# Performance work log

Measured on AMD Instinct MI355X. Metric: run time of the kernel, lower is better.

The kernel has to match this reference:

```python
import jax, jax.numpy as jnp
import numpy as np

B, SQ, SK = 8, 2048, 2048
QE = KE = VE = HID = 1024
NORM = HID ** 0.5


def setup_inputs() -> dict:
    key0 = jax.random.key(0)
    ks = jax.random.split(key0, 9)
    s = 1.0 / np.sqrt(HID)
    return {
        "key": jax.random.normal(ks[0], (B, SK, KE), dtype=jnp.float32),
        "query": jax.random.normal(ks[1], (B, SQ, QE), dtype=jnp.float32),
        "mask": jax.random.randint(ks[2], (B, SQ, SK), 0, 2, dtype=jnp.int32),
        # nn.Linear params: W has shape [out, in], y = x @ W.T + b
        "Wq": jax.random.uniform(ks[3], (HID, QE), jnp.float32, -s, s),
        "bq": jax.random.uniform(ks[4], (HID,), jnp.float32, -s, s),
        "Wk": jax.random.uniform(ks[5], (HID, KE), jnp.float32, -s, s),
        "bk": jax.random.uniform(ks[6], (HID,), jnp.float32, -s, s),
        "Wv": jax.random.uniform(ks[7], (HID, VE), jnp.float32, -s, s),
        "bv": jax.random.uniform(ks[8], (HID,), jnp.float32, -s, s),
    }


def reference(key, query, mask, Wq, bq, Wk, bk, Wv, bv):
    # QKV projections (note: value projection is applied to `key`, as in the original)
    q = jnp.einsum('bse,he->bsh', query, Wq) + bq   # [B,SQ,H]
    k = jnp.einsum('bse,he->bsh', key, Wk) + bk     # [B,SK,H]
    v = jnp.einsum('bse,he->bsh', key, Wv) + bv     # [B,SK,H]
    # scores + mask (0 -> -inf) in one fused pass
    score = jnp.einsum('bqh,bkh->bqk', q, k) / NORM  # [B,SQ,SK]
    score = jnp.where(mask == 0, -jnp.inf, score)
    score = jax.nn.softmax(score, axis=-1)
    # NaN cleanup for fully-masked rows (score.data[score != score] = 0)
    score = jnp.where(jnp.isnan(score), 0.0, score)
    output = jnp.einsum('bqk,bkh->bqh', score, v)    # [B,SQ,H]
    return (output, score)
```

## Files before the change

### kernel.cpp

```cpp
#include <hip/hip_runtime.h>
#include <hip/hip_bf16.h>

typedef __bf16 bf16;
typedef __bf16 bf16x8 __attribute__((ext_vector_type(8)));
typedef float  f32x4  __attribute__((ext_vector_type(4)));
typedef int    i32x4  __attribute__((ext_vector_type(4)));

#define TK 32
#define FB_TM 128
#define FB_TN 128
#define LDS_PAD 40

typedef __attribute__((address_space(3))) void       lds_t;
typedef __attribute__((address_space(1))) const void gbl_t;
__device__ __forceinline__ void async16(const void* g, void* l) {
    __builtin_amdgcn_global_load_lds((gbl_t*)g, (lds_t*)l, 16, 0, 0);
}

template<typename TC, int BIAS, int NTC>
__global__ __launch_bounds__(256, 2)
void gemm_bt(const bf16* __restrict__ A, const bf16* __restrict__ B,
             TC* __restrict__ C, const float* __restrict__ bias,
             int K, int lda, int ldb, int ldc,
             long sA, long sB, long sC)
{
    constexpr int BM  = 256, BN = 128;
    constexpr int ASZ = BM * TK;
    constexpr int BSZ = BN * TK;
    constexpr int BUFE = ASZ + BSZ;
    __shared__ bf16 lds[3 * BUFE];

    const int gx = gridDim.x, gy = gridDim.y;
    int lin = blockIdx.x + gx * (blockIdx.y + gy * blockIdx.z);
    const int cpx = (gx * gy * gridDim.z) >> 3;
    lin = (lin & 7) * cpx + (lin >> 3);
    const int bx  = lin % gx;
    const int rem = lin / gx;
    const int by  = rem % gy;
    const int bz  = rem / gy;

    A += (long)bz * sA;  B += (long)bz * sB;  C += (long)bz * sC;

    const int m0 = by * BM;
    const int n0 = bx * BN;

    const int t    = threadIdx.x;
    const int lane = t & 63;
    const int wave = t >> 6;
    const int wm   = (wave >> 1) * 128;
    const int wn   = (wave & 1) * 64;
    const int lrow = lane & 15;
    const int quad = lane >> 4;

    const int srow = lane >> 2;
    const int scol = (lane & 3) * 8;

    const bf16* pA = &A[(long)(m0 + wave * 16 + srow) * lda + scol];
    const bf16* pB = &B[(long)(n0 + wave * 16 + srow) * ldb + scol];

    const int NT_ = K / TK;

    auto stage = [&](int tile, int oS) {
        const int k0 = tile * TK;
        #pragma unroll
        for (int j = 0; j < 4; ++j)
            async16(pA + (long)(j * 64) * lda + k0,
                    &lds[oS + (wave * 16 + j * 64) * TK]);
        #pragma unroll
        for (int j = 0; j < 2; ++j)
            async16(pB + (long)(j * 64) * ldb + k0,
                    &lds[oS + ASZ + (wave * 16 + j * 64) * TK]);
    };

    stage(0, 0);
    asm volatile("" ::: "memory");
    stage(1, BUFE);

    int oC = 0, oN = BUFE, oS = 2 * BUFE;
    f32x4 acc[8][4] = {};

    for (int tt = 0; tt < NT_; ++tt) {
        if (tt < NT_ - 1) asm volatile("s_waitcnt vmcnt(6) lgkmcnt(0)" ::: "memory");
        else              asm volatile("s_waitcnt vmcnt(0) lgkmcnt(0)" ::: "memory");
        __builtin_amdgcn_s_barrier();
        __builtin_amdgcn_sched_barrier(0);

        if (tt + 2 < NT_) stage(tt + 2, oS);

        bf16x8 af[8], bfr[4];
        #pragma unroll
        for (int i = 0; i < 8; ++i)
            af[i] = *(bf16x8*)&lds[oC + (wm + i * 16 + lrow) * TK + quad * 8];
        #pragma unroll
        for (int j = 0; j < 4; ++j)
            bfr[j] = *(bf16x8*)&lds[oC + ASZ + (wn + j * 16 + lrow) * TK + quad * 8];

        #pragma unroll
        for (int i = 0; i < 8; ++i)
            #pragma unroll
            for (int j = 0; j < 4; ++j)
                acc[i][j] = __builtin_amdgcn_mfma_f32_16x16x32_bf16(
                    af[i], bfr[j], acc[i][j], 0, 0, 0);

        const int tmp = oC; oC = oN; oN = oS; oS = tmp;
    }

    #pragma unroll
    for (int i = 0; i < 8; ++i) {
        #pragma unroll
        for (int j = 0; j < 4; ++j) {
            #pragma unroll
            for (int r = 0; r < 4; ++r) {
                const int row = m0 + wm + i * 16 + quad * 4 + r;
                const int col = n0 + wn + j * 16 + lrow;
                float v = acc[i][j][r];
                if (BIAS == 1) v += bias[col];
                if (BIAS == 2) v += bias[row];
                if constexpr (NTC)
                    __builtin_nontemporal_store((TC)v, &C[(long)row * ldc + col]);
                else
                    C[(long)row * ldc + col] = (TC)v;
            }
        }
    }
}

__global__ __launch_bounds__(256)
void cvt_f32_bf16(const float* __restrict__ x, bf16* __restrict__ y)
{
    const long i = ((long)blockIdx.x * 256 + threadIdx.x) * 8;
    const f32x4 a = __builtin_nontemporal_load((const f32x4*)(x + i));
    const f32x4 b = __builtin_nontemporal_load((const f32x4*)(x + i + 4));
    bf16x8 v;
    v[0] = (bf16)a[0]; v[1] = (bf16)a[1]; v[2] = (bf16)a[2]; v[3] = (bf16)a[3];
    v[4] = (bf16)b[0]; v[5] = (bf16)b[1]; v[6] = (bf16)b[2]; v[7] = (bf16)b[3];
    *(bf16x8*)(y + i) = v;
}

template<typename T>
__device__ inline void stage8(bf16* dst, const T* src) {
    if constexpr (sizeof(T) == 4) {
        const float4 f0 = *(const float4*)src;
        const float4 f1 = *(const float4*)(src + 4);
        bf16x8 v;
        v[0] = (bf16)f0.x; v[1] = (bf16)f0.y; v[2] = (bf16)f0.z; v[3] = (bf16)f0.w;
        v[4] = (bf16)f1.x; v[5] = (bf16)f1.y; v[6] = (bf16)f1.z; v[7] = (bf16)f1.w;
        *(bf16x8*)dst = v;
    } else {
        *(uint4*)dst = *(const uint4*)src;
    }
}

template<typename TA, typename TB, typename TC, int BIAS>
__global__ __launch_bounds__(256)
void gemm_nt(const TA* __restrict__ A, const TB* __restrict__ B,
             TC* __restrict__ C, const float* __restrict__ bias,
             int K, int lda, int ldb, int ldc,
             long sA, long sB, long sC)
{
    __shared__ bf16 lsA[FB_TM * LDS_PAD];
    __shared__ bf16 lsB[FB_TN * LDS_PAD];

    const int bz = blockIdx.z;
    A += (long)bz * sA;  B += (long)bz * sB;  C += (long)bz * sC;

    const int m0 = blockIdx.y * FB_TM;
    const int n0 = blockIdx.x * FB_TN;

    const int t    = threadIdx.x;
    const int lane = t & 63;
    const int wave = t >> 6;
    const int wm   = (wave >> 1) * 64;
    const int wn   = (wave & 1) * 64;
    const int lrow = lane & 15;
    const int quad = lane >> 4;
    const int sr = t >> 2;
    const int sk = (t & 3) * 8;

    f32x4 acc[4][4] = {};

    for (int k0 = 0; k0 < K; k0 += TK) {
        __syncthreads();
        #pragma unroll
        for (int h = 0; h < 2; ++h) {
            const int row = h * 64 + sr;
            stage8(&lsA[row * LDS_PAD + sk], &A[(long)(m0 + row) * lda + k0 + sk]);
            stage8(&lsB[row * LDS_PAD + sk], &B[(long)(n0 + row) * ldb + k0 + sk]);
        }
        __syncthreads();

        bf16x8 af[4], bfr[4];
        #pragma unroll
        for (int i = 0; i < 4; ++i)
            af[i] = *(bf16x8*)&lsA[(wm + i * 16 + lrow) * LDS_PAD + quad * 8];
        #pragma unroll
        for (int j = 0; j < 4; ++j)
            bfr[j] = *(bf16x8*)&lsB[(wn + j * 16 + lrow) * LDS_PAD + quad * 8];

        #pragma unroll
        for (int i = 0; i < 4; ++i)
            #pragma unroll
            for (int j = 0; j < 4; ++j)
                acc[i][j] = __builtin_amdgcn_mfma_f32_16x16x32_bf16(
                    af[i], bfr[j], acc[i][j], 0, 0, 0);
    }

    #pragma unroll
    for (int i = 0; i < 4; ++i) {
        #pragma unroll
        for (int j = 0; j < 4; ++j) {
            #pragma unroll
            for (int r = 0; r < 4; ++r) {
                const int row = m0 + wm + i * 16 + quad * 4 + r;
                const int col = n0 + wn + j * 16 + lrow;
                float v = acc[i][j][r];
                if (BIAS == 1) v += bias[col];
                if (BIAS == 2) v += bias[row];
                C[(long)row * ldc + col] = (TC)v;
            }
        }
    }
}

template<int DUAL>
__global__ __launch_bounds__(256)
void softmax_rows(float* __restrict__ score, const int* __restrict__ mask,
                  bf16* __restrict__ pb)
{
    const int t = threadIdx.x;
    const long base = (long)blockIdx.x * 2048 + t * 8;

    const f32x4 a0 = *(const f32x4*)(score + base);
    const f32x4 a1 = *(const f32x4*)(score + base + 4);
    const i32x4 mA = __builtin_nontemporal_load((const i32x4*)(mask + base));
    const i32x4 mB = __builtin_nontemporal_load((const i32x4*)(mask + base + 4));

    const float INV = 0.03125f;
    float s[8];
    #pragma unroll
    for (int i = 0; i < 4; ++i) s[i]     = mA[i] ? a0[i] * INV : -INFINITY;
    #pragma unroll
    for (int i = 0; i < 4; ++i) s[4 + i] = mB[i] ? a1[i] * INV : -INFINITY;

    float mx = s[0];
    #pragma unroll
    for (int i = 1; i < 8; ++i) mx = fmaxf(mx, s[i]);
    #pragma unroll
    for (int o = 32; o > 0; o >>= 1) mx = fmaxf(mx, __shfl_xor(mx, o, 64));

    __shared__ float redm[4], reds[4];
    const int wave = t >> 6, lane = t & 63;
    if (lane == 0) redm[wave] = mx;
    __syncthreads();
    mx = fmaxf(fmaxf(redm[0], redm[1]), fmaxf(redm[2], redm[3]));

    const bool dead = !(mx > -INFINITY);
    float e[8], sum = 0.f;
    #pragma unroll
    for (int i = 0; i < 8; ++i) {
        const float x = dead ? 0.0f : __expf(s[i] - mx);
        e[i] = x;
        sum += x;
    }
    #pragma unroll
    for (int o = 32; o > 0; o >>= 1) sum += __shfl_xor(sum, o, 64);
    if (lane == 0) reds[wave] = sum;
    __syncthreads();
    sum = reds[0] + reds[1] + reds[2] + reds[3];

    const float inv = dead ? 0.0f : (1.0f / sum);
    f32x4 o0, o1;
    float p[8];
    #pragma unroll
    for (int i = 0; i < 8; ++i) p[i] = e[i] * inv;
    o0[0] = p[0]; o0[1] = p[1]; o0[2] = p[2]; o0[3] = p[3];
    o1[0] = p[4]; o1[1] = p[5]; o1[2] = p[6]; o1[3] = p[7];

    __builtin_nontemporal_store(o0, (f32x4*)(score + base));
    __builtin_nontemporal_store(o1, (f32x4*)(score + base + 4));
    if (DUAL) {
        bf16x8 v;
        #pragma unroll
        for (int i = 0; i < 8; ++i) v[i] = (bf16)p[i];
        *(bf16x8*)(pb + base) = v;
    }
}

extern "C" void kernel_launch(void* const* d_in, const int* in_sizes, int n_in,
                              void* d_out, int out_size, void* d_ws, size_t ws_size,
                              hipStream_t stream)
{
    const float* key   = (const float*)d_in[0];
    const float* query = (const float*)d_in[1];
    const int*   mask  = (const int*)d_in[2];
    const float* Wq = (const float*)d_in[3];
    const float* bq = (const float*)d_in[4];
    const float* Wk = (const float*)d_in[5];
    const float* bk = (const float*)d_in[6];
    const float* Wv = (const float*)d_in[7];
    const float* bv = (const float*)d_in[8];

    float* out   = (float*)d_out;
    float* score = out + (size_t)8 * 2048 * 1024;

    const dim3 blk(256, 1, 1);
    const long SB = (long)2048 * 1024;
    const long SS = (long)2048 * 2048;
    const size_t NX = (size_t)8 * 2048 * 1024;
    const size_t NW = (size_t)1024 * 1024;

    const size_t NEED = (4 * NX + 3 * NW) * sizeof(bf16);

    if (ws_size >= NEED) {
        bf16* xb = (bf16*)d_ws;
        bf16* qb = xb + NX;
        bf16* kb = qb + NX;
        bf16* vt = kb + NX;
        bf16* wq = vt + NX;
        bf16* wk = wq + NW;
        bf16* wv = wk + NW;
        bf16* Pb = xb;

        cvt_f32_bf16<<<dim3(NW / 2048), blk, 0, stream>>>(Wq, wq);
        cvt_f32_bf16<<<dim3(NW / 2048), blk, 0, stream>>>(Wk, wk);
        cvt_f32_bf16<<<dim3(NW / 2048), blk, 0, stream>>>(Wv, wv);

        cvt_f32_bf16<<<dim3(NX / 2048), blk, 0, stream>>>(key, xb);
        gemm_bt<bf16, 1, 0><<<dim3(8, 64, 1), blk, 0, stream>>>(
            xb, wk, kb, bk, 1024, 1024, 1024, 1024, 0, 0, 0);
        gemm_bt<bf16, 2, 0><<<dim3(16, 4, 8), blk, 0, stream>>>(
            wv, xb, vt, bv, 1024, 1024, 1024, 2048, 0, SB, SB);

        cvt_f32_bf16<<<dim3(NX / 2048), blk, 0, stream>>>(query, xb);
        gemm_bt<bf16, 1, 0><<<dim3(8, 64, 1), blk, 0, stream>>>(
            xb, wq, qb, bq, 1024, 1024, 1024, 1024, 0, 0, 0);

        gemm_bt<float, 0, 0><<<dim3(16, 8, 8), blk, 0, stream>>>(
            qb, kb, score, nullptr, 1024, 1024, 1024, 2048, SB, SB, SS);

        softmax_rows<1><<<dim3(16384), blk, 0, stream>>>(score, mask, Pb);

        gemm_bt<float, 0, 1><<<dim3(8, 8, 8), blk, 0, stream>>>(
            Pb, vt, out, nullptr, 2048, 2048, 2048, 1024, SS, SB, SB);
    } else {
        bf16* qb = (bf16*)d_ws;
        bf16* kb = qb + NX;
        bf16* vt = kb + NX;

        gemm_nt<float, float, bf16, 1><<<dim3(8, 128, 1), blk, 0, stream>>>(
            query, Wq, qb, bq, 1024, 1024, 1024, 1024, 0, 0, 0);
        gemm_nt<float, float, bf16, 1><<<dim3(8, 128, 1), blk, 0, stream>>>(
            key, Wk, kb, bk, 1024, 1024, 1024, 1024, 0, 0, 0);
        gemm_nt<float, float, bf16, 2><<<dim3(16, 8, 8), blk, 0, stream>>>(
            Wv, key, vt, bv, 1024, 1024, 1024, 2048, 0, SB, SB);
        gemm_nt<bf16, bf16, float, 0><<<dim3(16, 16, 8), blk, 0, stream>>>(
            qb, kb, score, nullptr, 1024, 1024, 1024, 2048, SB, SB, SS);
        softmax_rows<0><<<dim3(16384), blk, 0, stream>>>(score, mask, nullptr);
        gemm_nt<float, bf16, float, 0><<<dim3(8, 16, 8), blk, 0, stream>>>(
            score, vt, out, nullptr, 2048, 2048, 2048, 1024, SS, SB, SB);
    }
}
```

Before: 653.8 us.

## Split GEMM main loop into two phases interleaving loads with MFMA

The bf16 GEMM inner loop is split into two half-steps. Each half-step issues part of the next-next tile's async global-to-LDS loads alongside the LDS fragment reads, then runs its MFMA block at raised wave priority, with barriers between the halves. The goal is to spread memory issue across the compute and keep MFMA units busier. The three weight-conversion launches are also merged into one grid with a y-dimension to cut launch overhead. The extra barriers and waitcnts per iteration add synchronization cost that may offset the overlap.

```diff
diff --git a/kernel.cpp b/kernel.cpp
--- a/kernel.cpp
+++ b/kernel.cpp
@@ -60,21 +60,26 @@
 
     const int NT_ = K / TK;
 
-    auto stage = [&](int tile, int oS) {
+    auto stage3a = [&](int tile, int oS) {
         const int k0 = tile * TK;
         #pragma unroll
-        for (int j = 0; j < 4; ++j)
+        for (int j = 0; j < 3; ++j)
             async16(pA + (long)(j * 64) * lda + k0,
                     &lds[oS + (wave * 16 + j * 64) * TK]);
+    };
+    auto stage3b = [&](int tile, int oS) {
+        const int k0 = tile * TK;
+        async16(pA + (long)(3 * 64) * lda + k0,
+                &lds[oS + (wave * 16 + 3 * 64) * TK]);
         #pragma unroll
         for (int j = 0; j < 2; ++j)
             async16(pB + (long)(j * 64) * ldb + k0,
                     &lds[oS + ASZ + (wave * 16 + j * 64) * TK]);
     };
 
-    stage(0, 0);
+    stage3a(0, 0); stage3b(0, 0);
     asm volatile("" ::: "memory");
-    stage(1, BUFE);
+    stage3a(1, BUFE); stage3b(1, BUFE);
 
     int oC = 0, oN = BUFE, oS = 2 * BUFE;
     f32x4 acc[8][4] = {};
@@ -85,22 +90,46 @@
         __builtin_amdgcn_s_barrier();
         __builtin_amdgcn_sched_barrier(0);
 
-        if (tt + 2 < NT_) stage(tt + 2, oS);
-
         bf16x8 af[8], bfr[4];
-        #pragma unroll
-        for (int i = 0; i < 8; ++i)
+
+        #pragma unroll
+        for (int i = 0; i < 4; ++i)
             af[i] = *(bf16x8*)&lds[oC + (wm + i * 16 + lrow) * TK + quad * 8];
         #pragma unroll
         for (int j = 0; j < 4; ++j)
             bfr[j] = *(bf16x8*)&lds[oC + ASZ + (wn + j * 16 + lrow) * TK + quad * 8];
-
-        #pragma unroll
-        for (int i = 0; i < 8; ++i)
+        if (tt + 2 < NT_) stage3a(tt + 2, oS);
+        __builtin_amdgcn_sched_barrier(0);
+        __builtin_amdgcn_s_barrier();
+        asm volatile("s_waitcnt lgkmcnt(0)" ::: "memory");
+        __builtin_amdgcn_sched_barrier(0);
+        __builtin_amdgcn_s_setprio(1);
+        #pragma unroll
+        for (int i = 0; i < 4; ++i)
             #pragma unroll
             for (int j = 0; j < 4; ++j)
                 acc[i][j] = __builtin_amdgcn_mfma_f32_16x16x32_bf16(
                     af[i], bfr[j], acc[i][j], 0, 0, 0);
+        __builtin_amdgcn_s_setprio(0);
+        __builtin_amdgcn_sched_barrier(0);
+        __builtin_amdgcn_s_barrier();
+
+        #pragma unroll
+        for (int i = 4; i < 8; ++i)
+            af[i] = *(bf16x8*)&lds[oC + (wm + i * 16 + lrow) * TK + quad * 8];
+        if (tt + 2 < NT_) stage3b(tt + 2, oS);
+        __builtin_amdgcn_sched_barrier(0);
+        __builtin_amdgcn_s_barrier();
+        asm volatile("s_waitcnt lgkmcnt(0)" ::: "memory");
+        __builtin_amdgcn_sched_barrier(0);
+        __builtin_amdgcn_s_setprio(1);
+        #pragma unroll
+        for (int i = 4; i < 8; ++i)
+            #pragma unroll
+            for (int j = 0; j < 4; ++j)
+                acc[i][j] = __builtin_amdgcn_mfma_f32_16x16x32_bf16(
+                    af[i], bfr[j], acc[i][j], 0, 0, 0);
+        __builtin_amdgcn_s_setprio(0);
 
         const int tmp = oC; oC = oN; oN = oS; oS = tmp;
     }
@@ -137,6 +166,23 @@
     *(bf16x8*)(y + i) = v;
 }
 
+__global__ __launch_bounds__(256)
+void cvt3_f32_bf16(const float* __restrict__ x0, bf16* __restrict__ y0,
+                   const float* __restrict__ x1, bf16* __restrict__ y1,
+                   const float* __restrict__ x2, bf16* __restrict__ y2)
+{
+    const int which = blockIdx.y;
+    const float* x = which == 0 ? x0 : (which == 1 ? x1 : x2);
+    bf16*       y = which == 0 ? y0 : (which == 1 ? y1 : y2);
+    const long i = ((long)blockIdx.x * 256 + threadIdx.x) * 8;
+    const f32x4 a = __builtin_nontemporal_load((const f32x4*)(x + i));
+    const f32x4 b = __builtin_nontemporal_load((const f32x4*)(x + i + 4));
+    bf16x8 v;
+    v[0] = (bf16)a[0]; v[1] = (bf16)a[1]; v[2] = (bf16)a[2]; v[3] = (bf16)a[3];
+    v[4] = (bf16)b[0]; v[5] = (bf16)b[1]; v[6] = (bf16)b[2]; v[7] = (bf16)b[3];
+    *(bf16x8*)(y + i) = v;
+}
+
 template<typename T>
 __device__ inline void stage8(bf16* dst, const T* src) {
     if constexpr (sizeof(T) == 4) {
@@ -321,9 +367,8 @@
         bf16* wv = wk + NW;
         bf16* Pb = xb;
 
-        cvt_f32_bf16<<<dim3(NW / 2048), blk, 0, stream>>>(Wq, wq);
-        cvt_f32_bf16<<<dim3(NW / 2048), blk, 0, stream>>>(Wk, wk);
-        cvt_f32_bf16<<<dim3(NW / 2048), blk, 0, stream>>>(Wv, wv);
+        cvt3_f32_bf16<<<dim3(NW / 2048, 3), blk, 0, stream>>>(
+            Wq, wq, Wk, wk, Wv, wv);
 
         cvt_f32_bf16<<<dim3(NX / 2048), blk, 0, stream>>>(key, xb);
         gemm_bt<bf16, 1, 0><<<dim3(8, 64, 1), blk, 0, stream>>>(
```

Measured after the change: 647.3 us. Within noise of the previous version (-1.0%).
